# Performance work log

Hardware: AMD Instinct MI355X
Metric: run time of the kernel (lower is better)

The kernel has to match this reference:

```python
import jax, jax.numpy as jnp
import numpy as np

N_NODES = 100000
N_EDGES = 1600000
D_IN = 64
D_OUT = 64


def setup_inputs() -> dict:
    key = jax.random.key(0)
    ks = jax.random.split(key, 8)
    x = jax.random.normal(ks[0], (N_NODES, D_IN), dtype=jnp.float32)
    edge_rows = jax.random.randint(ks[1], (N_EDGES,), 0, N_NODES, dtype=jnp.int32)
    edge_cols = jax.random.randint(ks[2], (N_EDGES,), 0, N_NODES, dtype=jnp.int32)
    edge_vals = jax.random.uniform(ks[3], (N_EDGES,), dtype=jnp.float32)
    # xavier_uniform with gain=2.0: limit = gain * sqrt(6 / (fan_in + fan_out))
    lim = 2.0 * float(np.sqrt(6.0 / (D_IN + D_OUT)))
    weight_own = jax.random.uniform(ks[4], (D_IN, D_OUT), jnp.float32, -lim, lim)
    weight_nbr = jax.random.uniform(ks[5], (D_IN, D_OUT), jnp.float32, -lim, lim)
    weight_temp = jax.random.uniform(ks[6], (D_IN, D_OUT), jnp.float32, -lim, lim)
    bias = jnp.zeros((D_OUT,), jnp.float32)
    return {
        "x": x,
        "edge_rows": edge_rows,
        "edge_cols": edge_cols,
        "edge_vals": edge_vals,
        "weight_own": weight_own,
        "weight_nbr": weight_nbr,
        "weight_temp": weight_temp,
        "bias": bias,
    }


def _spmm(edge_rows, edge_cols, edge_vals, dense):
    # COO sparse [N,N] @ dense [N,D]: gather source rows, scale by edge value,
    # scatter-add into destination rows.
    msgs = edge_vals[:, None] * dense[edge_cols]  # [E, D]
    return jax.ops.segment_sum(msgs, edge_rows, num_segments=N_NODES)


def reference(x, edge_rows, edge_cols, edge_vals, weight_own, weight_nbr, weight_temp, bias):
    support = x @ weight_own    # [N, D_OUT]
    support1 = x @ weight_nbr
    support2 = x @ weight_temp
    output = _spmm(edge_rows, edge_cols, edge_vals, support)
    output1 = _spmm(edge_rows, edge_cols, edge_vals, support1)
    output2 = _spmm(edge_rows, edge_cols, edge_vals, support2)
    return output + output1 + output2 + bias
```

## Files before the change

### kernel.cpp

```cpp
#include <hip/hip_runtime.h>
#include <hip/hip_bf16.h>

#define D 64
#define RPB 256
#define RSH 8
#define NBMAX 1024
#define CPAD 16

__global__ __launch_bounds__(256) void gemm_kernel(const float* __restrict__ x,
                                                   const float* __restrict__ w0,
                                                   const float* __restrict__ w1,
                                                   const float* __restrict__ w2,
                                                   __hip_bfloat16* __restrict__ support,
                                                   int n) {
    __shared__ float Ws[D * D];
    __shared__ float xs[4][D];

    for (int i = threadIdx.x; i < D * D; i += 256)
        Ws[i] = w0[i] + w1[i] + w2[i];
    __syncthreads();

    const int wid  = threadIdx.x >> 6;
    const int lane = threadIdx.x & 63;
    int row = blockIdx.x * 4 + wid;
    const int nw = gridDim.x * 4;

    for (; row < n; row += nw) {
        xs[wid][lane] = x[(size_t)row * D + lane];
        float acc = 0.0f;
#pragma unroll
        for (int k = 0; k < D; ++k) {
            acc += xs[wid][k] * Ws[k * D + lane];
        }
        support[(size_t)row * D + lane] = __float2bfloat16(acc);
    }
}

__global__ __launch_bounds__(256) void gemm_f32_kernel(const float* __restrict__ x,
                                                       const float* __restrict__ w0,
                                                       const float* __restrict__ w1,
                                                       const float* __restrict__ w2,
                                                       float* __restrict__ support,
                                                       int n) {
    __shared__ float Ws[D * D];
    __shared__ float xs[4][D];
    for (int i = threadIdx.x; i < D * D; i += 256)
        Ws[i] = w0[i] + w1[i] + w2[i];
    __syncthreads();
    const int wid  = threadIdx.x >> 6;
    const int lane = threadIdx.x & 63;
    int row = blockIdx.x * 4 + wid;
    const int nw = gridDim.x * 4;
    for (; row < n; row += nw) {
        xs[wid][lane] = x[(size_t)row * D + lane];
        float acc = 0.0f;
#pragma unroll
        for (int k = 0; k < D; ++k) acc += xs[wid][k] * Ws[k * D + lane];
        support[(size_t)row * D + lane] = acc;
    }
}

__global__ __launch_bounds__(256) void zero_kernel(int* __restrict__ p, int n) {
    int i = blockIdx.x * 256 + threadIdx.x;
    int stride = gridDim.x * 256;
    for (; i < n; i += stride) p[i] = 0;
}

__global__ __launch_bounds__(256) void bucket_hist_kernel(const int* __restrict__ rows,
                                                          int ne, int* __restrict__ gcnt,
                                                          int nb) {
    __shared__ int lcnt[NBMAX];
    for (int i = threadIdx.x; i < nb; i += 256) lcnt[i] = 0;
    __syncthreads();
    int i = blockIdx.x * 256 + threadIdx.x;
    int stride = gridDim.x * 256;
    for (; i < ne; i += stride) atomicAdd(&lcnt[rows[i] >> RSH], 1);
    __syncthreads();
    for (int b = threadIdx.x; b < nb; b += 256) {
        int c = lcnt[b];
        if (c) atomicAdd(&gcnt[b * CPAD], c);
    }
}

__global__ __launch_bounds__(256) void bucket_scan_kernel(const int* __restrict__ gcnt,
                                                          int nb,
                                                          int* __restrict__ base,
                                                          int* __restrict__ cursor) {
    __shared__ int ts[256];
    const int tid = threadIdx.x;
    int b0 = tid * 4;
    int v[4]; int tsum = 0;
#pragma unroll
    for (int j = 0; j < 4; ++j) {
        int idx = b0 + j;
        v[j] = (idx < nb) ? gcnt[idx * CPAD] : 0;
        tsum += v[j];
    }
    ts[tid] = tsum;
    __syncthreads();
    for (int off = 1; off < 256; off <<= 1) {
        int t = (tid >= off) ? ts[tid - off] : 0;
        __syncthreads();
        ts[tid] += t;
        __syncthreads();
    }
    int excl = ts[tid] - tsum;
#pragma unroll
    for (int j = 0; j < 4; ++j) {
        int idx = b0 + j;
        if (idx < nb) { base[idx] = excl; cursor[idx * CPAD] = excl; }
        excl += v[j];
    }
    if (tid == 255) base[nb] = excl;
}

__global__ __launch_bounds__(256) void bin_scatter_kernel(const int* __restrict__ rows,
                                                          const int* __restrict__ cols,
                                                          const float* __restrict__ vals,
                                                          int ne,
                                                          int* __restrict__ cursor,
                                                          int nb,
                                                          int2* __restrict__ binned) {
    __shared__ int lcnt[NBMAX];
    __shared__ int lbase[NBMAX];
    const int tid = threadIdx.x;
    const int ce = (ne + gridDim.x - 1) / gridDim.x;
    const int e0 = blockIdx.x * ce;
    const int e1 = min(ne, e0 + ce);

    for (int i = tid; i < nb; i += 256) lcnt[i] = 0;
    __syncthreads();
    for (int e = e0 + tid; e < e1; e += 256) atomicAdd(&lcnt[rows[e] >> RSH], 1);
    __syncthreads();
    for (int b = tid; b < nb; b += 256) {
        int c = lcnt[b];
        lbase[b] = c ? atomicAdd(&cursor[b * CPAD], c) : 0;
    }
    __syncthreads();
    for (int i = tid; i < nb; i += 256) lcnt[i] = 0;
    __syncthreads();
    for (int e = e0 + tid; e < e1; e += 256) {
        int r = rows[e];
        int b = r >> RSH;
        int loc = atomicAdd(&lcnt[b], 1);
        int2 cv;
        cv.x = ((r & (RPB - 1)) << 17) | cols[e];
        cv.y = __float_as_int(vals[e]);
        binned[lbase[b] + loc] = cv;
    }
}

__global__ __launch_bounds__(512) void local_csr_kernel(const int* __restrict__ base,
                                                        const int2* __restrict__ binned,
                                                        int* __restrict__ rowptr,
                                                        int2* __restrict__ csr,
                                                        int n) {
    __shared__ int lh[RPB];
    __shared__ int lp[RPB];
    const int tid = threadIdx.x;
    const int b = blockIdx.x;
    const int jb = base[b], je = base[b + 1];

    for (int i = tid; i < RPB; i += 512) lh[i] = 0;
    __syncthreads();
    for (int j = jb + tid; j < je; j += 512) atomicAdd(&lh[binned[j].x >> 17], 1);
    __syncthreads();
    if (tid < RPB) lp[tid] = lh[tid];
    __syncthreads();
    for (int off = 1; off < RPB; off <<= 1) {
        int t = (tid < RPB && tid >= off) ? lp[tid - off] : 0;
        __syncthreads();
        if (tid < RPB) lp[tid] += t;
        __syncthreads();
    }
    if (tid < RPB) {
        int excl = lp[tid] - lh[tid];
        int start = jb + excl;
        lh[tid] = start;
        int r = b * RPB + tid;
        if (r < n) rowptr[r] = start;
    }
    __syncthreads();
    for (int j = jb + tid; j < je; j += 512) {
        int2 e = binned[j];
        int rl = e.x >> 17;
        int pos = atomicAdd(&lh[rl], 1);
        int2 o; o.x = e.x & 0x1FFFF; o.y = e.y;
        csr[pos] = o;
    }
}

__global__ __launch_bounds__(256) void pull2_kernel(const int* __restrict__ rowptr,
                                                    const int2* __restrict__ csr,
                                                    const unsigned int* __restrict__ sup32,
                                                    const float* __restrict__ bias,
                                                    float* __restrict__ out, int n) {
    const int tid  = threadIdx.x;
    const int lane = tid & 63;
    const int half = lane >> 5;
    const int sub  = lane & 31;
    const int wave = blockIdx.x * 4 + (tid >> 6);
    const int nwave = gridDim.x * 4;
    const float2 b2 = reinterpret_cast<const float2*>(bias)[sub];

    for (int w = wave; 2 * w < n; w += nwave) {
        const int r = 2 * w + half;
        float ax = 0.0f, ay = 0.0f;
        if (r < n) {
            int jb = rowptr[r], je = rowptr[r + 1];
            int j = jb;
            for (; j + 3 < je; j += 4) {
                int2 e0 = csr[j], e1 = csr[j + 1], e2 = csr[j + 2], e3 = csr[j + 3];
                unsigned int u0 = sup32[(size_t)e0.x * 32 + sub];
                unsigned int u1 = sup32[(size_t)e1.x * 32 + sub];
                unsigned int u2 = sup32[(size_t)e2.x * 32 + sub];
                unsigned int u3 = sup32[(size_t)e3.x * 32 + sub];
                float v0 = __int_as_float(e0.y), v1 = __int_as_float(e1.y);
                float v2 = __int_as_float(e2.y), v3 = __int_as_float(e3.y);
                ax += v0 * __uint_as_float(u0 << 16);
                ay += v0 * __uint_as_float(u0 & 0xffff0000u);
                ax += v1 * __uint_as_float(u1 << 16);
                ay += v1 * __uint_as_float(u1 & 0xffff0000u);
                ax += v2 * __uint_as_float(u2 << 16);
                ay += v2 * __uint_as_float(u2 & 0xffff0000u);
                ax += v3 * __uint_as_float(u3 << 16);
                ay += v3 * __uint_as_float(u3 & 0xffff0000u);
            }
            for (; j < je; ++j) {
                int2 e = csr[j];
                unsigned int u = sup32[(size_t)e.x * 32 + sub];
                float v = __int_as_float(e.y);
                ax += v * __uint_as_float(u << 16);
                ay += v * __uint_as_float(u & 0xffff0000u);
            }
            float2 o; o.x = ax + b2.x; o.y = ay + b2.y;
            reinterpret_cast<float2*>(out)[(size_t)r * 32 + sub] = o;
        }
    }
}

__global__ __launch_bounds__(256) void init_kernel(const float* __restrict__ bias,
                                                   float* __restrict__ out, int total4) {
    int i = blockIdx.x * 256 + threadIdx.x;
    int stride = gridDim.x * 256;
    for (; i < total4; i += stride) {
        int base4 = (i * 4) & (D - 1);
        float4 bv;
        bv.x = bias[base4 + 0]; bv.y = bias[base4 + 1];
        bv.z = bias[base4 + 2]; bv.w = bias[base4 + 3];
        reinterpret_cast<float4*>(out)[i] = bv;
    }
}

__global__ __launch_bounds__(256) void scatter_kernel(const int* __restrict__ rows,
                                                      const int* __restrict__ cols,
                                                      const float* __restrict__ vals,
                                                      const float* __restrict__ support,
                                                      float* __restrict__ out, int ne) {
    const int wid  = blockIdx.x * 4 + (threadIdx.x >> 6);
    const int lane = threadIdx.x & 63;
    const int nw = gridDim.x * 4;
    for (int e = wid; e < ne; e += nw) {
        const int r = rows[e];
        const int c = cols[e];
        const float v = vals[e];
        unsafeAtomicAdd(&out[(size_t)r * D + lane], v * support[(size_t)c * D + lane]);
    }
}

extern "C" void kernel_launch(void* const* d_in, const int* in_sizes, int n_in,
                              void* d_out, int out_size, void* d_ws, size_t ws_size,
                              hipStream_t stream) {
    const float* x         = (const float*)d_in[0];
    const int*   edge_rows = (const int*)d_in[1];
    const int*   edge_cols = (const int*)d_in[2];
    const float* edge_vals = (const float*)d_in[3];
    const float* w_own     = (const float*)d_in[4];
    const float* w_nbr     = (const float*)d_in[5];
    const float* w_temp    = (const float*)d_in[6];
    const float* bias      = (const float*)d_in[7];

    float* out = (float*)d_out;
    const int n_nodes = in_sizes[0] / D;
    const int n_edges = in_sizes[1];
    const int nb = (n_nodes + RPB - 1) / RPB;

    char* ws = (char*)d_ws;
    size_t off = 0;
    auto take = [&](size_t bytes) -> char* {
        char* p = ws + off;
        off = (off + bytes + 15) & ~(size_t)15;
        return p;
    };
    __hip_bfloat16* support = (__hip_bfloat16*)take((size_t)n_nodes * D * sizeof(__hip_bfloat16));
    int2* binned = (int2*)take((size_t)n_edges * sizeof(int2));
    int2* csr    = (int2*)take((size_t)n_edges * sizeof(int2));
    int*  rowptr = (int*) take((size_t)(n_nodes + 1) * sizeof(int));
    int*  gcnt   = (int*) take((size_t)nb * CPAD * sizeof(int));
    int*  base   = (int*) take((size_t)(nb + 1) * sizeof(int));
    int*  cursor = (int*) take((size_t)nb * CPAD * sizeof(int));
    const bool full_fits = (off <= ws_size) && (nb <= NBMAX) && (n_nodes <= (1 << 17));

    if (full_fits) {
        gemm_kernel<<<1024, 256, 0, stream>>>(x, w_own, w_nbr, w_temp, support, n_nodes);
        zero_kernel<<<32, 256, 0, stream>>>(gcnt, nb * CPAD);
        bucket_hist_kernel<<<512, 256, 0, stream>>>(edge_rows, n_edges, gcnt, nb);
        bucket_scan_kernel<<<1, 256, 0, stream>>>(gcnt, nb, base, cursor);
        bin_scatter_kernel<<<512, 256, 0, stream>>>(edge_rows, edge_cols, edge_vals,
                                                    n_edges, cursor, nb, binned);
        local_csr_kernel<<<nb, 512, 0, stream>>>(base, binned, rowptr, csr, n_nodes);
        hipMemcpyAsync(rowptr + n_nodes, base + nb, sizeof(int),
                       hipMemcpyDeviceToDevice, stream);
        pull2_kernel<<<2048, 256, 0, stream>>>(rowptr, csr, (const unsigned int*)support,
                                               bias, out, n_nodes);
    } else {
        float* support_f = (float*)d_ws;
        gemm_f32_kernel<<<1024, 256, 0, stream>>>(x, w_own, w_nbr, w_temp, support_f, n_nodes);
        int total4 = (n_nodes * D) / 4;
        int blocks = (total4 + 255) / 256; if (blocks > 2048) blocks = 2048;
        init_kernel<<<blocks, 256, 0, stream>>>(bias, out, total4);
        scatter_kernel<<<2048, 256, 0, stream>>>(edge_rows, edge_cols, edge_vals,
                                                 support_f, out, n_edges);
    }
}
```

Before: 139.2 us.

## Widen CSR build blocks, unroll pull gather by 8, memset counters

Swaps the zeroing kernel for hipMemsetAsync and doubles the block count of the bucket histogram. The local CSR build now uses 1024-thread blocks instead of 512. The pull kernel's main loop is unrolled from 4 to 8 edges, issuing eight gathers before the FMAs, with a 2-edge remainder loop and a single tail edge. The aim is more memory-level parallelism in the gather-bound SpMM and less per-block latency in preprocessing, at the cost of more registers and possible lower occupancy.

```diff
diff --git a/kernel.cpp b/kernel.cpp
--- a/kernel.cpp
+++ b/kernel.cpp
@@ -58,12 +58,6 @@
         for (int k = 0; k < D; ++k) acc += xs[wid][k] * Ws[k * D + lane];
         support[(size_t)row * D + lane] = acc;
     }
-}
-
-__global__ __launch_bounds__(256) void zero_kernel(int* __restrict__ p, int n) {
-    int i = blockIdx.x * 256 + threadIdx.x;
-    int stride = gridDim.x * 256;
-    for (; i < n; i += stride) p[i] = 0;
 }
 
 __global__ __launch_bounds__(256) void bucket_hist_kernel(const int* __restrict__ rows,
@@ -150,20 +144,20 @@
     }
 }
 
-__global__ __launch_bounds__(512) void local_csr_kernel(const int* __restrict__ base,
-                                                        const int2* __restrict__ binned,
-                                                        int* __restrict__ rowptr,
-                                                        int2* __restrict__ csr,
-                                                        int n) {
+__global__ __launch_bounds__(1024) void local_csr_kernel(const int* __restrict__ base,
+                                                         const int2* __restrict__ binned,
+                                                         int* __restrict__ rowptr,
+                                                         int2* __restrict__ csr,
+                                                         int n) {
     __shared__ int lh[RPB];
     __shared__ int lp[RPB];
     const int tid = threadIdx.x;
     const int b = blockIdx.x;
     const int jb = base[b], je = base[b + 1];
 
-    for (int i = tid; i < RPB; i += 512) lh[i] = 0;
-    __syncthreads();
-    for (int j = jb + tid; j < je; j += 512) atomicAdd(&lh[binned[j].x >> 17], 1);
+    for (int i = tid; i < RPB; i += 1024) lh[i] = 0;
+    __syncthreads();
+    for (int j = jb + tid; j < je; j += 1024) atomicAdd(&lh[binned[j].x >> 17], 1);
     __syncthreads();
     if (tid < RPB) lp[tid] = lh[tid];
     __syncthreads();
@@ -181,7 +175,7 @@
         if (r < n) rowptr[r] = start;
     }
     __syncthreads();
-    for (int j = jb + tid; j < je; j += 512) {
+    for (int j = jb + tid; j < je; j += 1024) {
         int2 e = binned[j];
         int rl = e.x >> 17;
         int pos = atomicAdd(&lh[rl], 1);
@@ -207,26 +201,34 @@
         const int r = 2 * w + half;
         float ax = 0.0f, ay = 0.0f;
         if (r < n) {
-            int jb = rowptr[r], je = rowptr[r + 1];
+            const int jb = rowptr[r], je = rowptr[r + 1];
             int j = jb;
-            for (; j + 3 < je; j += 4) {
-                int2 e0 = csr[j], e1 = csr[j + 1], e2 = csr[j + 2], e3 = csr[j + 3];
+            for (; j + 7 < je; j += 8) {
+                int2 e[8];
+#pragma unroll
+                for (int u = 0; u < 8; ++u) e[u] = csr[j + u];
+                unsigned int g[8];
+#pragma unroll
+                for (int u = 0; u < 8; ++u)
+                    g[u] = sup32[(size_t)e[u].x * 32 + sub];
+#pragma unroll
+                for (int u = 0; u < 8; ++u) {
+                    float v = __int_as_float(e[u].y);
+                    ax += v * __uint_as_float(g[u] << 16);
+                    ay += v * __uint_as_float(g[u] & 0xffff0000u);
+                }
+            }
+            for (; j + 1 < je; j += 2) {
+                int2 e0 = csr[j], e1 = csr[j + 1];
                 unsigned int u0 = sup32[(size_t)e0.x * 32 + sub];
                 unsigned int u1 = sup32[(size_t)e1.x * 32 + sub];
-                unsigned int u2 = sup32[(size_t)e2.x * 32 + sub];
-                unsigned int u3 = sup32[(size_t)e3.x * 32 + sub];
                 float v0 = __int_as_float(e0.y), v1 = __int_as_float(e1.y);
-                float v2 = __int_as_float(e2.y), v3 = __int_as_float(e3.y);
                 ax += v0 * __uint_as_float(u0 << 16);
                 ay += v0 * __uint_as_float(u0 & 0xffff0000u);
                 ax += v1 * __uint_as_float(u1 << 16);
                 ay += v1 * __uint_as_float(u1 & 0xffff0000u);
-                ax += v2 * __uint_as_float(u2 << 16);
-                ay += v2 * __uint_as_float(u2 & 0xffff0000u);
-                ax += v3 * __uint_as_float(u3 << 16);
-                ay += v3 * __uint_as_float(u3 & 0xffff0000u);
             }
-            for (; j < je; ++j) {
+            if (j < je) {
                 int2 e = csr[j];
                 unsigned int u = sup32[(size_t)e.x * 32 + sub];
                 float v = __int_as_float(e.y);
@@ -303,12 +305,12 @@
 
     if (full_fits) {
         gemm_kernel<<<1024, 256, 0, stream>>>(x, w_own, w_nbr, w_temp, support, n_nodes);
-        zero_kernel<<<32, 256, 0, stream>>>(gcnt, nb * CPAD);
-        bucket_hist_kernel<<<512, 256, 0, stream>>>(edge_rows, n_edges, gcnt, nb);
+        hipMemsetAsync(gcnt, 0, (size_t)nb * CPAD * sizeof(int), stream);
+        bucket_hist_kernel<<<1024, 256, 0, stream>>>(edge_rows, n_edges, gcnt, nb);
         bucket_scan_kernel<<<1, 256, 0, stream>>>(gcnt, nb, base, cursor);
         bin_scatter_kernel<<<512, 256, 0, stream>>>(edge_rows, edge_cols, edge_vals,
                                                     n_edges, cursor, nb, binned);
-        local_csr_kernel<<<nb, 512, 0, stream>>>(base, binned, rowptr, csr, n_nodes);
+        local_csr_kernel<<<nb, 1024, 0, stream>>>(base, binned, rowptr, csr, n_nodes);
         hipMemcpyAsync(rowptr + n_nodes, base + nb, sizeof(int),
                        hipMemcpyDeviceToDevice, stream);
         pull2_kernel<<<2048, 256, 0, stream>>>(rowptr, csr, (const unsigned int*)support,
```

New measurement: 145.8 us. 1.05x slower.
